# Performance work log

Measured on AMD Instinct MI355X. Metric: run time of the kernel, lower is better.

The kernel has to match this reference:

```python
import jax, jax.numpy as jnp
import numpy as np

WEIGHT = 1.0  # init kwarg `weight`


def setup_inputs() -> dict:
    key = jax.random.key(0)
    k1, k2, k3 = jax.random.split(key, 3)
    network_mesh = jax.random.normal(k1, (4, 3, 32, 16, 32), dtype=jnp.float32)
    pc = jax.random.normal(k2, (4, 3, 16384), dtype=jnp.float32)
    fem_mesh = jax.random.normal(k3, (4, 3, 32, 16, 32), dtype=jnp.float32)
    return {"network_mesh": network_mesh, "pc": pc, "fem_mesh": fem_mesh}


def reference(network_mesh, pc, fem_mesh):
    B = network_mesh.shape[0]
    # top surface: [B,3,X,Z] -> [B,3,X*Z] -> [B,N,3]
    top = network_mesh[:, :, :, -1, :].reshape(B, 3, -1).transpose(0, 2, 1)
    bottom = network_mesh[:, :, :, :-1, :]
    pcp = pc.transpose(0, 2, 1)  # [B,M,3]
    # squared pairwise distances [B,M,N] via ||a||^2 + ||b||^2 - 2 a.b
    sq = (jnp.sum(pcp * pcp, axis=-1)[:, :, None]
          + jnp.sum(top * top, axis=-1)[:, None, :]
          - 2.0 * jnp.einsum('bmd,bnd->bmn', pcp, top))
    # chamfer dist2: squared distance from each pc point to nearest top point
    dist2 = jnp.min(sq, axis=-1)  # [B,M]
    fem_loss = jnp.mean((bottom - fem_mesh[:, :, :, :-1, :]) ** 2)
    return jnp.mean(dist2) + fem_loss * WEIGHT
```

## Files before the change

kernel.cpp:

```cpp
#include <hip/hip_runtime.h>
#include <hip/hip_bf16.h>
#include <float.h>


#define B_BATCH        4
#define MPTS           16384
#define NTOP           1024
#define NM_BATCH_STRIDE 49152
#define CH_STRIDE      16384

#define PC_PER_THREAD  8
#define PC_CHUNK       2048
#define N_CHUNKS       8
#define N_TILES        16
#define TILE_TOPS      64

#define NUM_DIST_BLOCKS (B_BATCH * N_CHUNKS * N_TILES)
#define NUM_FEM_BLOCKS  64
#define TOTAL_BLOCKS    (NUM_DIST_BLOCKS + NUM_FEM_BLOCKS)

#define TOTAL_M        65536
#define FEM_VEC4       46080

#define WS_BSUM  (N_TILES * TOTAL_M)
#define WS_FEM   (WS_BSUM + 256)

__device__ __forceinline__ float block_reduce_sum(float v) {
    for (int o = 32; o > 0; o >>= 1) v += __shfl_down(v, o, 64);
    __shared__ float s[4];
    int lane = threadIdx.x & 63;
    int w    = threadIdx.x >> 6;
    if (lane == 0) s[w] = v;
    __syncthreads();
    if (threadIdx.x == 0) v = s[0] + s[1] + s[2] + s[3];
    return v;
}

__global__ __launch_bounds__(256) void meshloss_partials(
    const float* __restrict__ nm,
    const float* __restrict__ pc,
    const float* __restrict__ fem,
    float* __restrict__ ws)
{
    const int t = threadIdx.x;

    if (blockIdx.x < NUM_DIST_BLOCKS) {
        __shared__ float4 top[TILE_TOPS];
        const int bid   = blockIdx.x;
        const int b     = bid >> 7;
        const int rem   = bid & 127;
        const int chunk = rem >> 4;
        const int tile  = rem & 15;

        const float* nmb = nm + b * NM_BATCH_STRIDE;
        if (t < TILE_TOPS) {
            const int p = tile * TILE_TOPS + t;
            const int i = p >> 5, k = p & 31;
            const int base = i * 512 + 480 + k;
            float x = nmb[0 * CH_STRIDE + base];
            float y = nmb[1 * CH_STRIDE + base];
            float z = nmb[2 * CH_STRIDE + base];
            top[t] = make_float4(x, y, z, x * x + y * y + z * z);
        }
        __syncthreads();

        const float* pcb = pc + b * NM_BATCH_STRIDE;
        const int mbase = chunk * PC_CHUNK + t;

        float px2[PC_PER_THREAD], py2[PC_PER_THREAD], pz2[PC_PER_THREAD];
        float pp[PC_PER_THREAD], mn[PC_PER_THREAD];
        #pragma unroll
        for (int j = 0; j < PC_PER_THREAD; ++j) {
            const int m = mbase + j * 256;
            float x = pcb[m];
            float y = pcb[CH_STRIDE + m];
            float z = pcb[2 * CH_STRIDE + m];
            pp[j]  = x * x + y * y + z * z;
            px2[j] = -2.0f * x;
            py2[j] = -2.0f * y;
            pz2[j] = -2.0f * z;
            mn[j]  = FLT_MAX;
        }

        #pragma unroll 2
        for (int n = 0; n < TILE_TOPS; n += 2) {
            float4 T0 = top[n];
            float4 T1 = top[n + 1];
            #pragma unroll
            for (int j = 0; j < PC_PER_THREAD; ++j) {
                float d0 = __builtin_fmaf(px2[j], T0.x,
                           __builtin_fmaf(py2[j], T0.y,
                           __builtin_fmaf(pz2[j], T0.z, T0.w)));
                float d1 = __builtin_fmaf(px2[j], T1.x,
                           __builtin_fmaf(py2[j], T1.y,
                           __builtin_fmaf(pz2[j], T1.z, T1.w)));
                mn[j] = fminf(mn[j], fminf(d0, d1));
            }
        }

        float* wrow = ws + tile * TOTAL_M + b * MPTS;
        #pragma unroll
        for (int j = 0; j < PC_PER_THREAD; ++j)
            wrow[mbase + j * 256] = mn[j] + pp[j];
    } else {
        const int fb = blockIdx.x - NUM_DIST_BLOCKS;
        const float4* nm4  = reinterpret_cast<const float4*>(nm);
        const float4* fem4 = reinterpret_cast<const float4*>(fem);
        float acc = 0.0f;
        for (int q = fb * 256 + t; q < FEM_VEC4; q += NUM_FEM_BLOCKS * 256) {
            const int bci = q / 120;
            const int r   = q - bci * 120;
            const int s   = bci * 128 + r;
            float4 a = nm4[s];
            float4 f = fem4[s];
            float dx = a.x - f.x, dy = a.y - f.y, dz = a.z - f.z, dw = a.w - f.w;
            acc += dx * dx + dy * dy + dz * dz + dw * dw;
        }
        float s = block_reduce_sum(acc);
        if (t == 0) ws[WS_FEM + fb] = s;
    }
}

__global__ __launch_bounds__(256) void meshloss_minreduce(
    const float* __restrict__ ws_in, float* __restrict__ ws)
{
    const int i = blockIdx.x * 256 + threadIdx.x;
    float v = ws_in[i];
    #pragma unroll
    for (int tl = 1; tl < N_TILES; ++tl)
        v = fminf(v, ws_in[tl * TOTAL_M + i]);
    float s = block_reduce_sum(v);
    if (threadIdx.x == 0) ws[WS_BSUM + blockIdx.x] = s;
}

__global__ __launch_bounds__(256) void meshloss_final(
    const float* __restrict__ ws, float* __restrict__ out)
{
    const int t = threadIdx.x;
    float v = ws[WS_BSUM + t] * (1.0f / 65536.0f);
    if (t < NUM_FEM_BLOCKS) v += ws[WS_FEM + t] * (1.0f / 184320.0f);
    v = block_reduce_sum(v);
    if (t == 0) out[0] = v;
}

extern "C" void kernel_launch(void* const* d_in, const int* in_sizes, int n_in,
                              void* d_out, int out_size, void* d_ws, size_t ws_size,
                              hipStream_t stream) {
    const float* nm  = (const float*)d_in[0];
    const float* pc  = (const float*)d_in[1];
    const float* fem = (const float*)d_in[2];
    float* out = (float*)d_out;
    float* ws  = (float*)d_ws;

    meshloss_partials<<<TOTAL_BLOCKS, 256, 0, stream>>>(nm, pc, fem, ws);
    meshloss_minreduce<<<256, 256, 0, stream>>>(ws, ws);
    meshloss_final<<<1, 256, 0, stream>>>(ws, out);
}
```

Measured before the change: 17.18 us.

## Fuse final reduction into min-reduce kernel with atomics, move FEM loss there, retile distances

The three-kernel pipeline becomes two. The FEM squared-error sum moves out of the distance kernel into the reduction kernel, and the separate single-block final kernel is replaced by per-block atomicAdd into the output, which the distance kernel zeroes first. The distance tiling also changes to 8 tiles of 128 top points with 4 points per thread and 16 chunks, which halves the intermediate workspace the reduction has to read. This saves one launch and some traffic, at the cost of a nondeterministic float atomic summation order and heavier per-block work in the reduction.

```diff
diff --git a/kernel.cpp b/kernel.cpp
--- a/kernel.cpp
+++ b/kernel.cpp
@@ -3,27 +3,22 @@
 #include <float.h>
 
 
-#define B_BATCH        4
-#define MPTS           16384
-#define NTOP           1024
+#define B_BATCH         4
+#define MPTS            16384
 #define NM_BATCH_STRIDE 49152
-#define CH_STRIDE      16384
+#define CH_STRIDE       16384
 
-#define PC_PER_THREAD  8
-#define PC_CHUNK       2048
-#define N_CHUNKS       8
-#define N_TILES        16
-#define TILE_TOPS      64
+#define PC_PER_THREAD   4
+#define PC_CHUNK        1024
+#define N_CHUNKS        16
+#define N_TILES         8
+#define TILE_TOPS       128
 
 #define NUM_DIST_BLOCKS (B_BATCH * N_CHUNKS * N_TILES)
-#define NUM_FEM_BLOCKS  64
-#define TOTAL_BLOCKS    (NUM_DIST_BLOCKS + NUM_FEM_BLOCKS)
+#define NUM_RED_BLOCKS  128
 
-#define TOTAL_M        65536
-#define FEM_VEC4       46080
-
-#define WS_BSUM  (N_TILES * TOTAL_M)
-#define WS_FEM   (WS_BSUM + 256)
+#define TOTAL_M         65536
+#define FEM_VEC4        46080
 
 __device__ __forceinline__ float block_reduce_sum(float v) {
     for (int o = 32; o > 0; o >>= 1) v += __shfl_down(v, o, 64);
@@ -36,111 +31,118 @@
     return v;
 }
 
-__global__ __launch_bounds__(256) void meshloss_partials(
+__global__ __launch_bounds__(256) void meshloss_dist(
     const float* __restrict__ nm,
     const float* __restrict__ pc,
-    const float* __restrict__ fem,
-    float* __restrict__ ws)
+    float* __restrict__ ws,
+    float* __restrict__ out)
 {
-    const int t = threadIdx.x;
+    const int t   = threadIdx.x;
+    const int bid = blockIdx.x;
 
-    if (blockIdx.x < NUM_DIST_BLOCKS) {
-        __shared__ float4 top[TILE_TOPS];
-        const int bid   = blockIdx.x;
-        const int b     = bid >> 7;
-        const int rem   = bid & 127;
-        const int chunk = rem >> 4;
-        const int tile  = rem & 15;
+    if (bid == 0 && t == 0) out[0] = 0.0f;
 
-        const float* nmb = nm + b * NM_BATCH_STRIDE;
-        if (t < TILE_TOPS) {
-            const int p = tile * TILE_TOPS + t;
-            const int i = p >> 5, k = p & 31;
-            const int base = i * 512 + 480 + k;
-            float x = nmb[0 * CH_STRIDE + base];
-            float y = nmb[1 * CH_STRIDE + base];
-            float z = nmb[2 * CH_STRIDE + base];
-            top[t] = make_float4(x, y, z, x * x + y * y + z * z);
-        }
-        __syncthreads();
+    const int b     = bid >> 7;
+    const int rem   = bid & 127;
+    const int chunk = rem >> 3;
+    const int tile  = rem & 7;
 
-        const float* pcb = pc + b * NM_BATCH_STRIDE;
-        const int mbase = chunk * PC_CHUNK + t;
+    __shared__ float4 top[TILE_TOPS];
+    const float* nmb = nm + b * NM_BATCH_STRIDE;
+    if (t < TILE_TOPS) {
+        const int p = tile * TILE_TOPS + t;
+        const int i = p >> 5, k = p & 31;
+        const int base = i * 512 + 480 + k;
+        float x = nmb[0 * CH_STRIDE + base];
+        float y = nmb[1 * CH_STRIDE + base];
+        float z = nmb[2 * CH_STRIDE + base];
+        top[t] = make_float4(x, y, z, x * x + y * y + z * z);
+    }
+    __syncthreads();
 
-        float px2[PC_PER_THREAD], py2[PC_PER_THREAD], pz2[PC_PER_THREAD];
-        float pp[PC_PER_THREAD], mn[PC_PER_THREAD];
+    const float* pcb = pc + b * NM_BATCH_STRIDE;
+    const int mbase = chunk * PC_CHUNK + t;
+
+    float px2[PC_PER_THREAD], py2[PC_PER_THREAD], pz2[PC_PER_THREAD];
+    float pp[PC_PER_THREAD], mn[PC_PER_THREAD];
+    #pragma unroll
+    for (int j = 0; j < PC_PER_THREAD; ++j) {
+        const int m = mbase + j * 256;
+        float x = pcb[m];
+        float y = pcb[CH_STRIDE + m];
+        float z = pcb[2 * CH_STRIDE + m];
+        pp[j]  = x * x + y * y + z * z;
+        px2[j] = -2.0f * x;
+        py2[j] = -2.0f * y;
+        pz2[j] = -2.0f * z;
+        mn[j]  = FLT_MAX;
+    }
+
+    for (int n = 0; n < TILE_TOPS; n += 4) {
+        float4 T0 = top[n + 0];
+        float4 T1 = top[n + 1];
+        float4 T2 = top[n + 2];
+        float4 T3 = top[n + 3];
         #pragma unroll
         for (int j = 0; j < PC_PER_THREAD; ++j) {
-            const int m = mbase + j * 256;
-            float x = pcb[m];
-            float y = pcb[CH_STRIDE + m];
-            float z = pcb[2 * CH_STRIDE + m];
-            pp[j]  = x * x + y * y + z * z;
-            px2[j] = -2.0f * x;
-            py2[j] = -2.0f * y;
-            pz2[j] = -2.0f * z;
-            mn[j]  = FLT_MAX;
+            float d0 = __builtin_fmaf(px2[j], T0.x,
+                       __builtin_fmaf(py2[j], T0.y,
+                       __builtin_fmaf(pz2[j], T0.z, T0.w)));
+            float d1 = __builtin_fmaf(px2[j], T1.x,
+                       __builtin_fmaf(py2[j], T1.y,
+                       __builtin_fmaf(pz2[j], T1.z, T1.w)));
+            float d2 = __builtin_fmaf(px2[j], T2.x,
+                       __builtin_fmaf(py2[j], T2.y,
+                       __builtin_fmaf(pz2[j], T2.z, T2.w)));
+            float d3 = __builtin_fmaf(px2[j], T3.x,
+                       __builtin_fmaf(py2[j], T3.y,
+                       __builtin_fmaf(pz2[j], T3.z, T3.w)));
+            mn[j] = fminf(mn[j], fminf(d0, d1));
+            mn[j] = fminf(mn[j], fminf(d2, d3));
         }
+    }
 
-        #pragma unroll 2
-        for (int n = 0; n < TILE_TOPS; n += 2) {
-            float4 T0 = top[n];
-            float4 T1 = top[n + 1];
-            #pragma unroll
-            for (int j = 0; j < PC_PER_THREAD; ++j) {
-                float d0 = __builtin_fmaf(px2[j], T0.x,
-                           __builtin_fmaf(py2[j], T0.y,
-                           __builtin_fmaf(pz2[j], T0.z, T0.w)));
-                float d1 = __builtin_fmaf(px2[j], T1.x,
-                           __builtin_fmaf(py2[j], T1.y,
-                           __builtin_fmaf(pz2[j], T1.z, T1.w)));
-                mn[j] = fminf(mn[j], fminf(d0, d1));
-            }
-        }
-
-        float* wrow = ws + tile * TOTAL_M + b * MPTS;
-        #pragma unroll
-        for (int j = 0; j < PC_PER_THREAD; ++j)
-            wrow[mbase + j * 256] = mn[j] + pp[j];
-    } else {
-        const int fb = blockIdx.x - NUM_DIST_BLOCKS;
-        const float4* nm4  = reinterpret_cast<const float4*>(nm);
-        const float4* fem4 = reinterpret_cast<const float4*>(fem);
-        float acc = 0.0f;
-        for (int q = fb * 256 + t; q < FEM_VEC4; q += NUM_FEM_BLOCKS * 256) {
-            const int bci = q / 120;
-            const int r   = q - bci * 120;
-            const int s   = bci * 128 + r;
-            float4 a = nm4[s];
-            float4 f = fem4[s];
-            float dx = a.x - f.x, dy = a.y - f.y, dz = a.z - f.z, dw = a.w - f.w;
-            acc += dx * dx + dy * dy + dz * dz + dw * dw;
-        }
-        float s = block_reduce_sum(acc);
-        if (t == 0) ws[WS_FEM + fb] = s;
-    }
+    float* wrow = ws + tile * TOTAL_M + b * MPTS;
+    #pragma unroll
+    for (int j = 0; j < PC_PER_THREAD; ++j)
+        wrow[mbase + j * 256] = mn[j] + pp[j];
 }
 
-__global__ __launch_bounds__(256) void meshloss_minreduce(
-    const float* __restrict__ ws_in, float* __restrict__ ws)
+__global__ __launch_bounds__(256) void meshloss_reduce(
+    const float* __restrict__ ws,
+    const float* __restrict__ nm,
+    const float* __restrict__ fem,
+    float* __restrict__ out)
 {
-    const int i = blockIdx.x * 256 + threadIdx.x;
-    float v = ws_in[i];
+    const int gid = blockIdx.x * 256 + threadIdx.x;
+
+    float dsum = 0.0f;
     #pragma unroll
-    for (int tl = 1; tl < N_TILES; ++tl)
-        v = fminf(v, ws_in[tl * TOTAL_M + i]);
+    for (int h = 0; h < 2; ++h) {
+        const int p = gid + h * 32768;
+        float v = ws[p];
+        #pragma unroll
+        for (int tl = 1; tl < N_TILES; ++tl)
+            v = fminf(v, ws[tl * TOTAL_M + p]);
+        dsum += v;
+    }
+
+    const float4* nm4  = reinterpret_cast<const float4*>(nm);
+    const float4* fem4 = reinterpret_cast<const float4*>(fem);
+    float fsum = 0.0f;
+    for (int q = gid; q < FEM_VEC4; q += NUM_RED_BLOCKS * 256) {
+        const int bci = q / 120;
+        const int r   = q - bci * 120;
+        const int s   = bci * 128 + r;
+        float4 a = nm4[s];
+        float4 f = fem4[s];
+        float dx = a.x - f.x, dy = a.y - f.y, dz = a.z - f.z, dw = a.w - f.w;
+        fsum += dx * dx + dy * dy + dz * dz + dw * dw;
+    }
+
+    float v = dsum * (1.0f / 65536.0f) + fsum * (1.0f / 184320.0f);
     float s = block_reduce_sum(v);
-    if (threadIdx.x == 0) ws[WS_BSUM + blockIdx.x] = s;
-}
-
-__global__ __launch_bounds__(256) void meshloss_final(
-    const float* __restrict__ ws, float* __restrict__ out)
-{
-    const int t = threadIdx.x;
-    float v = ws[WS_BSUM + t] * (1.0f / 65536.0f);
-    if (t < NUM_FEM_BLOCKS) v += ws[WS_FEM + t] * (1.0f / 184320.0f);
-    v = block_reduce_sum(v);
-    if (t == 0) out[0] = v;
+    if (threadIdx.x == 0) atomicAdd(out, s);
 }
 
 extern "C" void kernel_launch(void* const* d_in, const int* in_sizes, int n_in,
@@ -152,7 +154,6 @@
     float* out = (float*)d_out;
     float* ws  = (float*)d_ws;
 
-    meshloss_partials<<<TOTAL_BLOCKS, 256, 0, stream>>>(nm, pc, fem, ws);
-    meshloss_minreduce<<<256, 256, 0, stream>>>(ws, ws);
-    meshloss_final<<<1, 256, 0, stream>>>(ws, out);
+    meshloss_dist<<<NUM_DIST_BLOCKS, 256, 0, stream>>>(nm, pc, ws, out);
+    meshloss_reduce<<<NUM_RED_BLOCKS, 256, 0, stream>>>(ws, nm, fem, out);
 }
```

Measured after the change: 16.18 us. 1.06x faster.
